# Kernel optimization log

Measured on AMD Instinct MI355X. Metric: run time of the kernel, lower is better.

The kernel has to match this reference:

```python
import jax, jax.numpy as jnp
import numpy as np

N_NODES = 100000
N_EDGES = 1600000
IN_SIZE = 512
HID_SIZE = 256
OUT_SIZE = 16
DROP_P = 0.5


def _degrees(idx, n):
    d = jax.ops.segment_sum(jnp.ones(idx.shape[0], jnp.float32), idx, num_segments=n)
    return jnp.maximum(d, 1.0)  # DGL clamps zero degrees to 1


def graph_conv(src, dst, feat, W, b, activation=None):
    # DGL GraphConv, norm='both': D_in^{-1/2} A D_out^{-1/2} X W + b
    n = feat.shape[0]
    inv_sqrt_dout = _degrees(src, n) ** -0.5   # out-degree of source nodes
    inv_sqrt_din = _degrees(dst, n) ** -0.5    # in-degree of destination nodes
    h = feat * inv_sqrt_dout[:, None]
    h = h @ W  # in_feats >= out_feats -> transform before aggregation (same math)
    # message passing: scatter-add source messages to destinations
    h = jax.ops.segment_sum(h[src], dst, num_segments=n)
    h = h * inv_sqrt_din[:, None] + b
    if activation is not None:
        h = activation(h)
    return h


def setup_inputs() -> dict:
    key = jax.random.key(0)
    ks = jax.random.split(key, 9)
    features = jax.random.normal(ks[0], (N_NODES, IN_SIZE), jnp.float32)
    src = jax.random.randint(ks[1], (N_EDGES,), 0, N_NODES)
    dst = jax.random.randint(ks[2], (N_EDGES,), 0, N_NODES)
    W1 = jax.random.normal(ks[3], (IN_SIZE, HID_SIZE), jnp.float32) / np.sqrt(IN_SIZE).astype(np.float32)
    b1 = jnp.zeros((HID_SIZE,), jnp.float32)
    W2 = jax.random.normal(ks[4], (HID_SIZE, HID_SIZE), jnp.float32) / np.sqrt(HID_SIZE).astype(np.float32)
    b2 = jnp.zeros((HID_SIZE,), jnp.float32)
    W3 = jax.random.normal(ks[5], (HID_SIZE, OUT_SIZE), jnp.float32) / np.sqrt(HID_SIZE).astype(np.float32)
    b3 = jnp.zeros((OUT_SIZE,), jnp.float32)
    return {"features": features, "src": src, "dst": dst,
            "W1": W1, "b1": b1, "W2": W2, "b2": b2, "W3": W3, "b3": b3}


def reference(features, src, dst, W1, b1, W2, b2, W3, b3):
    # layer 0: GraphConv + relu
    h = graph_conv(src, dst, features, W1, b1, activation=jax.nn.relu)
    # dropout(0.5) before layer 1 (deterministic fixed-key mask, training semantics)
    keep = jax.random.bernoulli(jax.random.key(42), 1.0 - DROP_P, h.shape)
    h = jnp.where(keep, h / (1.0 - DROP_P), 0.0)
    # layer 1: GraphConv (no activation)
    h = graph_conv(src, dst, h, W2, b2, activation=None)
    # layer 2: plain Linear head
    return h @ W3 + b3
```

## Files before the change

kernel.cpp:

```cpp
#include <hip/hip_runtime.h>
#include <stdint.h>

#define NN    100000
#define NE    1600000
#define IN_F  512
#define HID   256
#define OUTF  16
#define NPAD  100096
#define NBK   391
#define EPB   8192

typedef unsigned int u32;
typedef __bf16 bfrag  __attribute__((ext_vector_type(8)));
typedef float  f32x4  __attribute__((ext_vector_type(4)));
typedef short  s16x8  __attribute__((ext_vector_type(8)));

__device__ __forceinline__ u32 rotl32(u32 x, int r){ return (x<<r)|(x>>(32-r)); }

__device__ __forceinline__ bool drop_keep(u32 i){
    const u32 ks0 = 0u, ks1 = 42u, ks2 = 0x1BD11BDAu ^ 0u ^ 42u;
    u32 x0 = 0u + ks0;
    u32 x1 = i  + ks1;
#define TFR(r) { x0 += x1; x1 = rotl32(x1,(r)); x1 ^= x0; }
    TFR(13) TFR(15) TFR(26) TFR(6)   x0 += ks1; x1 += ks2 + 1u;
    TFR(17) TFR(29) TFR(16) TFR(24)  x0 += ks2; x1 += ks0 + 2u;
    TFR(13) TFR(15) TFR(26) TFR(6)   x0 += ks0; x1 += ks1 + 3u;
    TFR(17) TFR(29) TFR(16) TFR(24)  x0 += ks1; x1 += ks2 + 4u;
    TFR(13) TFR(15) TFR(26) TFR(6)   x0 += ks2; x1 += ks0 + 5u;
#undef TFR
    return ((x0 ^ x1) >> 31) == 0u;
}

__device__ __forceinline__ short f2b(float f){
    union { float f; u32 u; } v; v.f = f;
    u32 r = (v.u + 0x7FFFu + ((v.u >> 16) & 1u)) >> 16;
    return (short)r;
}
__device__ __forceinline__ float blo(u32 u){ union{u32 u; float f;} v; v.u = u << 16;         return v.f; }
__device__ __forceinline__ float bhi(u32 u){ union{u32 u; float f;} v; v.u = u & 0xFFFF0000u; return v.f; }

__device__ __forceinline__ u32 cvt_pk_bf16(float lo, float hi){
    u32 r;
    asm("v_cvt_pk_bf16_f32 %0, %1, %2" : "=v"(r) : "v"(lo), "v"(hi));
    return r;
}

__device__ __forceinline__ void gll16(const void* g, void* l){
    __builtin_amdgcn_global_load_lds((const __attribute__((address_space(1))) void*)g,
                                     (__attribute__((address_space(3))) void*)l, 16, 0, 0);
}


__global__ __launch_bounds__(256) void build_hist(const int4* __restrict__ src4,
                                                  const int4* __restrict__ dst4,
                                                  int* deg_out, int* __restrict__ bcnt){
    __shared__ int h[NBK];
    int t = threadIdx.x;
    for (int i = t; i < NBK; i += 256) h[i] = 0;
    __syncthreads();
    for (int i = blockIdx.x * 256 + t; i < NE / 4; i += gridDim.x * 256) {
        int4 s = src4[i];
        int4 d = dst4[i];
        atomicAdd(&deg_out[s.x], 1);
        atomicAdd(&deg_out[s.y], 1);
        atomicAdd(&deg_out[s.z], 1);
        atomicAdd(&deg_out[s.w], 1);
        atomicAdd(&h[d.x >> 8], 1);
        atomicAdd(&h[d.y >> 8], 1);
        atomicAdd(&h[d.z >> 8], 1);
        atomicAdd(&h[d.w >> 8], 1);
    }
    __syncthreads();
    for (int i = t; i < NBK; i += 256)
        if (h[i]) atomicAdd(&bcnt[i], h[i]);
}

__global__ __launch_bounds__(256) void finalize_deg(const int* __restrict__ deg_out,
                                                    const int* __restrict__ row_ptr,
                                                    float* isdo, float* isdi){
    int i = blockIdx.x * blockDim.x + threadIdx.x;
    if (i < NN) {
        isdo[i] = rsqrtf(fmaxf((float)deg_out[i], 1.0f));
        isdi[i] = rsqrtf(fmaxf((float)(row_ptr[i + 1] - row_ptr[i]), 1.0f));
    }
}

__global__ __launch_bounds__(512) void bucket_scan(const int* __restrict__ bcnt,
                                                   int* __restrict__ bbase,
                                                   int* __restrict__ bcur,
                                                   int* __restrict__ row_ptr){
    __shared__ int sh[512];
    int t = threadIdx.x;
    int v = (t < NBK) ? bcnt[t] : 0;
    sh[t] = v;
    __syncthreads();
    for (int off = 1; off < 512; off <<= 1) {
        int a = (t >= off) ? sh[t - off] : 0;
        __syncthreads();
        sh[t] += a;
        __syncthreads();
    }
    int excl = sh[t] - v;
    if (t < NBK) { bbase[t] = excl; bcur[t] = excl; }
    if (t == 0)  { bbase[NBK] = NE; row_ptr[NN] = NE; }
}

__global__ __launch_bounds__(256) void bucket_scatter(const int* __restrict__ src,
                                                      const int* __restrict__ dst,
                                                      int* bcur, u32* __restrict__ tmp){
    __shared__ int lh[NBK];
    __shared__ int lb[NBK];
    int t = threadIdx.x;
    for (int i = t; i < NBK; i += 256) lh[i] = 0;
    __syncthreads();
    const int e0 = blockIdx.x * EPB;
    for (int k = t * 4; k < EPB; k += 1024) {
        int e = e0 + k;
        if (e < NE) {
            int4 d = *(const int4*)(dst + e);
            atomicAdd(&lh[d.x >> 8], 1);
            atomicAdd(&lh[d.y >> 8], 1);
            atomicAdd(&lh[d.z >> 8], 1);
            atomicAdd(&lh[d.w >> 8], 1);
        }
    }
    __syncthreads();
    for (int i = t; i < NBK; i += 256) {
        int c = lh[i];
        if (c) lb[i] = atomicAdd(&bcur[i], c);
        lh[i] = 0;
    }
    __syncthreads();
    for (int k = t * 4; k < EPB; k += 1024) {
        int e = e0 + k;
        if (e < NE) {
            int4 d = *(const int4*)(dst + e);
            int4 s = *(const int4*)(src + e);
            int b0 = d.x >> 8, b1 = d.y >> 8, b2 = d.z >> 8, b3 = d.w >> 8;
            int r0 = atomicAdd(&lh[b0], 1);
            tmp[lb[b0] + r0] = ((u32)s.x << 8) | ((u32)d.x & 255u);
            int r1 = atomicAdd(&lh[b1], 1);
            tmp[lb[b1] + r1] = ((u32)s.y << 8) | ((u32)d.y & 255u);
            int r2 = atomicAdd(&lh[b2], 1);
            tmp[lb[b2] + r2] = ((u32)s.z << 8) | ((u32)d.z & 255u);
            int r3 = atomicAdd(&lh[b3], 1);
            tmp[lb[b3] + r3] = ((u32)s.w << 8) | ((u32)d.w & 255u);
        }
    }
}

__global__ __launch_bounds__(256) void bucket_finalize(const u32* __restrict__ tmp,
                                                       const int* __restrict__ bbase,
                                                       int* __restrict__ row_ptr,
                                                       int* __restrict__ col_src){
    __shared__ int h[256];
    __shared__ int wtot[4];
    const int t = threadIdx.x;
    const int b = blockIdx.x;
    const int base = bbase[b];
    const int cnt  = bbase[b + 1] - base;
    h[t] = 0;
    __syncthreads();
    for (int k = t; k < cnt; k += 256)
        atomicAdd(&h[tmp[base + k] & 255u], 1);
    __syncthreads();
    int v = h[t];
    int lane = t & 63, w = t >> 6;
    int s = v;
    #pragma unroll
    for (int off = 1; off < 64; off <<= 1) {
        int u = __shfl_up(s, off);
        if (lane >= off) s += u;
    }
    if (lane == 63) wtot[w] = s;
    __syncthreads();
    int woff = 0;
    #pragma unroll
    for (int i = 0; i < 4; ++i) woff += (i < w) ? wtot[i] : 0;
    int excl = woff + s - v;
    int d = (b << 8) + t;
    if (d < NN) row_ptr[d] = base + excl;
    h[t] = excl;
    __syncthreads();
    for (int k = t; k < cnt; k += 256) {
        u32 p = tmp[base + k];
        int r = atomicAdd(&h[p & 255u], 1);
        col_src[base + r] = (int)(p >> 8);
    }
}


template<int Kd, int Nd>
__global__ __launch_bounds__(256) void convert_wt(const float* __restrict__ W,
                                                  short* __restrict__ WT){
    int i = blockIdx.x * 256 + threadIdx.x;
    if (i >= Kd * Nd) return;
    int n = i / Kd, k = i - n * Kd;
    WT[i] = f2b(W[(size_t)k * Nd + n]);
}

__global__ __launch_bounds__(256) void gemm_x(const float* __restrict__ X,
                                              const short* __restrict__ BT,
                                              const float* __restrict__ isdo,
                                              short* __restrict__ C){
    __shared__ __align__(16) float As[4096];
    __shared__ __align__(16) short Bs[4096];

    const int t = threadIdx.x;
    const int wave = t >> 6, lane = t & 63;
    const int bm = blockIdx.x * 128;
    const int bn = blockIdx.y * 128;

    const int gsw = lane ^ ((lane >> 3) & 7);
    const int rl  = gsw >> 1;
    const int pp  = gsw & 1;
    const float* pa0 = X + (size_t)(((bm + 0*32 + rl) < NN) ? (bm + 0*32 + rl) : 0) * IN_F + wave * 8 + pp * 4;
    const float* pa1 = X + (size_t)(((bm + 1*32 + rl) < NN) ? (bm + 1*32 + rl) : 0) * IN_F + wave * 8 + pp * 4;
    const float* pa2 = X + (size_t)(((bm + 2*32 + rl) < NN) ? (bm + 2*32 + rl) : 0) * IN_F + wave * 8 + pp * 4;
    const float* pa3 = X + (size_t)(((bm + 3*32 + rl) < NN) ? (bm + 3*32 + rl) : 0) * IN_F + wave * 8 + pp * 4;
    float* lA = As + wave * 1024;

    const int ch0 = wave * 128 + lane;
    const int ch1 = ch0 + 64;
    const int kb0 = ch0 >> 7, r0 = ch0 & 127;
    const int kb1 = ch1 >> 7, r1 = ch1 & 127;
    const short* pb0 = BT + (size_t)(bn + r0) * IN_F + kb0 * 8;
    const short* pb1 = BT + (size_t)(bn + r1) * IN_F + kb1 * 8;
    short* lB0 = Bs + (size_t)(wave * 128) * 8;
    short* lB1 = Bs + (size_t)(wave * 128 + 64) * 8;

    const int wr = (wave >> 1) * 64, wc = (wave & 1) * 64;
    const int kq = lane >> 4, r15 = lane & 15;
    const short* fb = Bs + (size_t)(kq * 128 + wc + r15) * 8;

    f32x4 acc[4][4];
    #pragma unroll
    for (int m = 0; m < 4; ++m)
        #pragma unroll
        for (int n = 0; n < 4; ++n) acc[m][n] = (f32x4)0.0f;

    for (int k0 = 0; k0 < IN_F; k0 += 32) {
        gll16(pa0 + k0, lA);
        gll16(pa1 + k0, lA + 256);
        gll16(pa2 + k0, lA + 512);
        gll16(pa3 + k0, lA + 768);
        gll16(pb0 + k0, lB0);
        gll16(pb1 + k0, lB1);
        __syncthreads();

        bfrag af[4], bfg[4];
        #pragma unroll
        for (int m = 0; m < 4; ++m) {
            int r  = wr + m * 16 + r15;
            int j  = r >> 5, rr = r & 31;
            int g0 = 2 * rr;
            int G0 = g0 ^ ((g0 >> 3) & 7);
            int g1 = g0 + 1;
            int G1 = g1 ^ ((g1 >> 3) & 7);
            const float* base = As + kq * 1024 + j * 256;
            float4 f0 = *(const float4*)(base + G0 * 4);
            float4 f1 = *(const float4*)(base + G1 * 4);
            uint4 q = make_uint4(cvt_pk_bf16(f0.x, f0.y), cvt_pk_bf16(f0.z, f0.w),
                                 cvt_pk_bf16(f1.x, f1.y), cvt_pk_bf16(f1.z, f1.w));
            af[m] = *(bfrag*)&q;
        }
        #pragma unroll
        for (int n = 0; n < 4; ++n) bfg[n] = *(const bfrag*)(fb + n * 128);
        #pragma unroll
        for (int m = 0; m < 4; ++m)
            #pragma unroll
            for (int n = 0; n < 4; ++n)
                acc[m][n] = __builtin_amdgcn_mfma_f32_16x16x32_bf16(af[m], bfg[n], acc[m][n], 0, 0, 0);
        __syncthreads();
    }

    const int crow0 = bm + wr + (lane >> 4) * 4;
    const int ccol0 = bn + wc + (lane & 15);
    #pragma unroll
    for (int m = 0; m < 4; ++m)
        #pragma unroll
        for (int r = 0; r < 4; ++r) {
            int row = crow0 + m * 16 + r;
            float sc = (row < NN) ? isdo[row] : 0.0f;
            #pragma unroll
            for (int n = 0; n < 4; ++n)
                C[(size_t)row * HID + ccol0 + n * 16] = f2b(acc[m][n][r] * sc);
        }
}

template<int K>
__global__ __launch_bounds__(256) void gemm_bt(const short* __restrict__ A,
                                               const short* __restrict__ BT,
                                               short* __restrict__ C){
    __shared__ __align__(16) short As[4096];
    __shared__ __align__(16) short Bs[4096];

    const int t = threadIdx.x;
    const int wave = t >> 6, lane = t & 63;
    const int bm = blockIdx.x * 128;
    const int bn = blockIdx.y * 128;

    const int ch0 = wave * 128 + lane;
    const int ch1 = ch0 + 64;
    const int kb0 = ch0 >> 7, r0 = ch0 & 127;
    const int kb1 = ch1 >> 7, r1 = ch1 & 127;
    const short* pa0 = A  + (size_t)(bm + r0) * K + kb0 * 8;
    const short* pa1 = A  + (size_t)(bm + r1) * K + kb1 * 8;
    const short* pb0 = BT + (size_t)(bn + r0) * K + kb0 * 8;
    const short* pb1 = BT + (size_t)(bn + r1) * K + kb1 * 8;
    short* lA0 = As + (size_t)(wave * 128) * 8;
    short* lA1 = As + (size_t)(wave * 128 + 64) * 8;
    short* lB0 = Bs + (size_t)(wave * 128) * 8;
    short* lB1 = Bs + (size_t)(wave * 128 + 64) * 8;

    const int wr = (wave >> 1) * 64, wc = (wave & 1) * 64;
    const short* fa = As + (size_t)((lane >> 4) * 128 + wr + (lane & 15)) * 8;
    const short* fb = Bs + (size_t)((lane >> 4) * 128 + wc + (lane & 15)) * 8;

    f32x4 acc[4][4];
    #pragma unroll
    for (int m = 0; m < 4; ++m)
        #pragma unroll
        for (int n = 0; n < 4; ++n) acc[m][n] = (f32x4)0.0f;

    for (int k0 = 0; k0 < K; k0 += 32) {
        gll16(pa0 + k0, lA0);
        gll16(pa1 + k0, lA1);
        gll16(pb0 + k0, lB0);
        gll16(pb1 + k0, lB1);
        __syncthreads();

        bfrag af[4], bfg[4];
        #pragma unroll
        for (int m = 0; m < 4; ++m) af[m]  = *(const bfrag*)(fa + m * 128);
        #pragma unroll
        for (int n = 0; n < 4; ++n) bfg[n] = *(const bfrag*)(fb + n * 128);
        #pragma unroll
        for (int m = 0; m < 4; ++m)
            #pragma unroll
            for (int n = 0; n < 4; ++n)
                acc[m][n] = __builtin_amdgcn_mfma_f32_16x16x32_bf16(af[m], bfg[n], acc[m][n], 0, 0, 0);
        __syncthreads();
    }

    const int crow0 = bm + wr + (lane >> 4) * 4;
    const int ccol0 = bn + wc + (lane & 15);
    #pragma unroll
    for (int m = 0; m < 4; ++m)
        #pragma unroll
        for (int n = 0; n < 4; ++n)
            #pragma unroll
            for (int r = 0; r < 4; ++r)
                C[(size_t)(crow0 + m * 16 + r) * HID + ccol0 + n * 16] = f2b(acc[m][n][r]);
}

template<int MODE>
__global__ __launch_bounds__(256) void gather_agg(const short* __restrict__ H,
                                                  const int* __restrict__ rp,
                                                  const int* __restrict__ cs,
                                                  const float* __restrict__ isdi,
                                                  const float* __restrict__ isdo,
                                                  const float* __restrict__ bias,
                                                  short* __restrict__ out){
    const int lane = threadIdx.x & 63;
    const int node = __builtin_amdgcn_readfirstlane((int)(blockIdx.x * 4) + (int)(threadIdx.x >> 6));
    const int e0  = rp[node];
    const int end = rp[node + 1];
    const int sub = lane & 31, half = lane >> 5;
    const u32 off16 = (u32)sub * 16u;
    const char* Hb = (const char*)H;

    float a[8] = {0,0,0,0,0,0,0,0};
    float b[8] = {0,0,0,0,0,0,0,0};

#define LD4(s) (*(const uint4*)(Hb + ((((u32)(s)) << 9) | off16)))
#define ACC(A, u) { A[0]+=blo(u.x); A[1]+=bhi(u.x); A[2]+=blo(u.y); A[3]+=bhi(u.y); \
                    A[4]+=blo(u.z); A[5]+=bhi(u.z); A[6]+=blo(u.w); A[7]+=bhi(u.w); }

    int eb = e0;
    for (; eb + 16 <= end; eb += 16) {
        int t0 = cs[eb+0],  t1 = cs[eb+1],  t2 = cs[eb+2],  t3 = cs[eb+3];
        int t4 = cs[eb+4],  t5 = cs[eb+5],  t6 = cs[eb+6],  t7 = cs[eb+7];
        int t8 = cs[eb+8],  t9 = cs[eb+9],  tA = cs[eb+10], tB = cs[eb+11];
        int tC = cs[eb+12], tD = cs[eb+13], tE = cs[eb+14], tF = cs[eb+15];
        int s0 = half ? t1 : t0;
        int s1 = half ? t3 : t2;
        int s2 = half ? t5 : t4;
        int s3 = half ? t7 : t6;
        int s4 = half ? t9 : t8;
        int s5 = half ? tB : tA;
        int s6 = half ? tD : tC;
        int s7 = half ? tF : tE;
        uint4 u0 = LD4(s0), u1 = LD4(s1), u2 = LD4(s2), u3 = LD4(s3);
        uint4 u4 = LD4(s4), u5 = LD4(s5), u6 = LD4(s6), u7 = LD4(s7);
        ACC(a, u0); ACC(b, u1); ACC(a, u2); ACC(b, u3);
        ACC(a, u4); ACC(b, u5); ACC(a, u6); ACC(b, u7);
    }
    for (; eb + 8 <= end; eb += 8) {
        int t0 = cs[eb+0], t1 = cs[eb+1], t2 = cs[eb+2], t3 = cs[eb+3];
        int t4 = cs[eb+4], t5 = cs[eb+5], t6 = cs[eb+6], t7 = cs[eb+7];
        int s0 = half ? t1 : t0;
        int s1 = half ? t3 : t2;
        int s2 = half ? t5 : t4;
        int s3 = half ? t7 : t6;
        uint4 u0 = LD4(s0), u1 = LD4(s1), u2 = LD4(s2), u3 = LD4(s3);
        ACC(a, u0); ACC(b, u1); ACC(a, u2); ACC(b, u3);
    }
    for (; eb + 2 <= end; eb += 2) {
        int t0 = cs[eb], t1 = cs[eb+1];
        int s = half ? t1 : t0;
        uint4 u = LD4(s);
        ACC(a, u);
    }
    if (eb < end) {
        int s = cs[eb];
        uint4 u = LD4(s);
        if (half == 0) { ACC(a, u); }
    }
#undef ACC
#undef LD4
    #pragma unroll
    for (int j = 0; j < 8; ++j) a[j] += b[j];

    const int srcl = lane >> 1;
    const bool oddq = (lane & 1) != 0;
    float v[4];
    #pragma unroll
    for (int j = 0; j < 4; ++j) {
        float p0 = __shfl(a[j],     srcl);
        float p1 = __shfl(a[j + 4], srcl);
        float q0 = __shfl(a[j],     srcl + 32);
        float q1 = __shfl(a[j + 4], srcl + 32);
        v[j] = oddq ? (p1 + q1) : (p0 + q0);
    }

    float sd = isdi[node];
    float4 bb = *(const float4*)(bias + lane * 4);
    float h0 = v[0] * sd + bb.x;
    float h1 = v[1] * sd + bb.y;
    float h2 = v[2] * sd + bb.z;
    float h3 = v[3] * sd + bb.w;

    if (MODE == 0) {
        float so2 = 2.0f * isdo[node];
        u32 base = (u32)node * HID + (u32)lane * 4;
        h0 = drop_keep(base + 0) ? fmaxf(h0, 0.f) * so2 : 0.f;
        h1 = drop_keep(base + 1) ? fmaxf(h1, 0.f) * so2 : 0.f;
        h2 = drop_keep(base + 2) ? fmaxf(h2, 0.f) * so2 : 0.f;
        h3 = drop_keep(base + 3) ? fmaxf(h3, 0.f) * so2 : 0.f;
    }

    uint2 wv;
    wv.x = ((u32)(unsigned short)f2b(h1) << 16) | (u32)(unsigned short)f2b(h0);
    wv.y = ((u32)(unsigned short)f2b(h3) << 16) | (u32)(unsigned short)f2b(h2);
    *(uint2*)((char*)out + (size_t)node * 512 + (u32)lane * 8u) = wv;
}

__global__ __launch_bounds__(256) void head_kernel(const short* __restrict__ H2,
                                                   const float* __restrict__ W3,
                                                   const float* __restrict__ b3,
                                                   float* __restrict__ out){
    __shared__ float W3s[HID * OUTF];
    __shared__ short rows[16][HID + 8];
    int t = threadIdx.x;
    for (int i = t; i < HID * OUTF; i += 256) W3s[i] = W3[i];
    const int n0 = blockIdx.x * 16;
    for (int c = t; c < 16 * 32; c += 256) {
        int r = c >> 5, cc = c & 31;
        *(s16x8*)(&rows[r][cc * 8]) = *(const s16x8*)(H2 + (size_t)(n0 + r) * HID + cc * 8);
    }
    __syncthreads();
    int nl = t >> 4, k = t & 15;
    float acc = 0.0f;
    #pragma unroll 4
    for (int j = 0; j < HID; ++j)
        acc += blo((u32)(unsigned short)rows[nl][j]) * W3s[j * OUTF + k];
    out[(size_t)(n0 + nl) * OUTF + k] = acc + b3[k];
}

extern "C" void kernel_launch(void* const* d_in, const int* in_sizes, int n_in,
                              void* d_out, int out_size, void* d_ws, size_t ws_size,
                              hipStream_t stream) {
    const float* X   = (const float*)d_in[0];
    const int*   src = (const int*)  d_in[1];
    const int*   dst = (const int*)  d_in[2];
    const float* W1  = (const float*)d_in[3];
    const float* b1  = (const float*)d_in[4];
    const float* W2  = (const float*)d_in[5];
    const float* b2  = (const float*)d_in[6];
    const float* W3  = (const float*)d_in[7];
    const float* b3  = (const float*)d_in[8];
    float* out = (float*)d_out;

    char* ws = (char*)d_ws;
    size_t o = 0;
    int*   deg_out = (int*)  (ws + o); o += (size_t)NN * 4;
    int*   bcnt    = (int*)  (ws + o); o += (size_t)NBK * 4;
    float* isdo    = (float*)(ws + o); o += (size_t)NN * 4;
    float* isdi    = (float*)(ws + o); o += (size_t)NN * 4;
    int*   row_ptr = (int*)  (ws + o); o += (size_t)(NN + 1) * 4;
    int*   bbase   = (int*)  (ws + o); o += (size_t)(NBK + 1) * 4;
    int*   bcur    = (int*)  (ws + o); o += (size_t)NBK * 4;
    int*   col_src = (int*)  (ws + o); o += (size_t)NE * 4;
    o = (o + 255) & ~(size_t)255;
    short* W1t = (short*)(ws + o); o += (size_t)IN_F * HID * 2;
    short* W2t = (short*)(ws + o); o += (size_t)HID * HID * 2;
    o = (o + 255) & ~(size_t)255;
    short* hA    = (short*)(ws + o); o += (size_t)NPAD * HID * 2;
    short* hB    = (short*)(ws + o); o += (size_t)NPAD * HID * 2;
    short* h2pre = (short*)(ws + o); o += (size_t)NPAD * HID * 2;
    if (ws_size < o) return;
    short* h2  = hA;
    u32*   tmp = (u32*)hB;

    const size_t zlen = (size_t)NN * 4 + (size_t)NBK * 4;
    hipMemsetAsync(deg_out, 0, zlen, stream);

    build_hist<<<256, 256, 0, stream>>>((const int4*)src, (const int4*)dst, deg_out, bcnt);
    bucket_scan<<<1, 512, 0, stream>>>(bcnt, bbase, bcur, row_ptr);
    bucket_scatter<<<(NE + EPB - 1) / EPB, 256, 0, stream>>>(src, dst, bcur, tmp);
    bucket_finalize<<<NBK, 256, 0, stream>>>(tmp, bbase, row_ptr, col_src);
    finalize_deg<<<(NN + 255) / 256, 256, 0, stream>>>(deg_out, row_ptr, isdo, isdi);

    convert_wt<IN_F, HID><<<IN_F * HID / 256, 256, 0, stream>>>(W1, W1t);
    convert_wt<HID, HID><<<HID * HID / 256, 256, 0, stream>>>(W2, W2t);

    dim3 ggrid(NPAD / 128, 2);

    gemm_x<<<ggrid, 256, 0, stream>>>(X, W1t, isdo, hA);
    gather_agg<0><<<NN / 4, 256, 0, stream>>>(hA, row_ptr, col_src, isdi, isdo, b1, hB);

    gemm_bt<HID><<<ggrid, 256, 0, stream>>>(hB, W2t, h2pre);
    gather_agg<1><<<NN / 4, 256, 0, stream>>>(h2pre, row_ptr, col_src, isdi, isdo, b2, h2);

    head_kernel<<<NN / 16, 256, 0, stream>>>(h2, W3, b3, out);
}
```

Measured before the change: 535.7 us.

## Double-buffer LDS tiles in both GEMM kernels to overlap loads with MFMA

Both GEMM kernels now use two LDS buffers. The next K-tile's global-to-LDS loads are issued before the current tile is computed, and a partial vmcnt wait plus raw barriers replace the full __syncthreads. The goal is to hide global load latency behind the MFMA work. In exchange, LDS use per block doubles (48KB for gemm_x), which may reduce occupancy, and correctness depends on the hand-written vmcnt counts matching the number of outstanding loads.

New measurement: 538.3 us. Within noise of the previous version (+0.5%).

```diff
diff --git a/kernel.cpp b/kernel.cpp
--- a/kernel.cpp
+++ b/kernel.cpp
@@ -203,8 +203,8 @@
                                               const short* __restrict__ BT,
                                               const float* __restrict__ isdo,
                                               short* __restrict__ C){
-    __shared__ __align__(16) float As[4096];
-    __shared__ __align__(16) short Bs[4096];
+    __shared__ __align__(16) float As[2 * 4096];
+    __shared__ __align__(16) short Bs[2 * 4096];
 
     const int t = threadIdx.x;
     const int wave = t >> 6, lane = t & 63;
@@ -218,7 +218,6 @@
     const float* pa1 = X + (size_t)(((bm + 1*32 + rl) < NN) ? (bm + 1*32 + rl) : 0) * IN_F + wave * 8 + pp * 4;
     const float* pa2 = X + (size_t)(((bm + 2*32 + rl) < NN) ? (bm + 2*32 + rl) : 0) * IN_F + wave * 8 + pp * 4;
     const float* pa3 = X + (size_t)(((bm + 3*32 + rl) < NN) ? (bm + 3*32 + rl) : 0) * IN_F + wave * 8 + pp * 4;
-    float* lA = As + wave * 1024;
 
     const int ch0 = wave * 128 + lane;
     const int ch1 = ch0 + 64;
@@ -226,12 +225,9 @@
     const int kb1 = ch1 >> 7, r1 = ch1 & 127;
     const short* pb0 = BT + (size_t)(bn + r0) * IN_F + kb0 * 8;
     const short* pb1 = BT + (size_t)(bn + r1) * IN_F + kb1 * 8;
-    short* lB0 = Bs + (size_t)(wave * 128) * 8;
-    short* lB1 = Bs + (size_t)(wave * 128 + 64) * 8;
 
     const int wr = (wave >> 1) * 64, wc = (wave & 1) * 64;
     const int kq = lane >> 4, r15 = lane & 15;
-    const short* fb = Bs + (size_t)(kq * 128 + wc + r15) * 8;
 
     f32x4 acc[4][4];
     #pragma unroll
@@ -239,40 +235,56 @@
         #pragma unroll
         for (int n = 0; n < 4; ++n) acc[m][n] = (f32x4)0.0f;
 
-    for (int k0 = 0; k0 < IN_F; k0 += 32) {
-        gll16(pa0 + k0, lA);
-        gll16(pa1 + k0, lA + 256);
-        gll16(pa2 + k0, lA + 512);
-        gll16(pa3 + k0, lA + 768);
-        gll16(pb0 + k0, lB0);
-        gll16(pb1 + k0, lB1);
-        __syncthreads();
-
-        bfrag af[4], bfg[4];
-        #pragma unroll
-        for (int m = 0; m < 4; ++m) {
-            int r  = wr + m * 16 + r15;
-            int j  = r >> 5, rr = r & 31;
-            int g0 = 2 * rr;
-            int G0 = g0 ^ ((g0 >> 3) & 7);
-            int g1 = g0 + 1;
-            int G1 = g1 ^ ((g1 >> 3) & 7);
-            const float* base = As + kq * 1024 + j * 256;
-            float4 f0 = *(const float4*)(base + G0 * 4);
-            float4 f1 = *(const float4*)(base + G1 * 4);
-            uint4 q = make_uint4(cvt_pk_bf16(f0.x, f0.y), cvt_pk_bf16(f0.z, f0.w),
-                                 cvt_pk_bf16(f1.x, f1.y), cvt_pk_bf16(f1.z, f1.w));
-            af[m] = *(bfrag*)&q;
-        }
-        #pragma unroll
-        for (int n = 0; n < 4; ++n) bfg[n] = *(const bfrag*)(fb + n * 128);
-        #pragma unroll
-        for (int m = 0; m < 4; ++m)
-            #pragma unroll
-            for (int n = 0; n < 4; ++n)
-                acc[m][n] = __builtin_amdgcn_mfma_f32_16x16x32_bf16(af[m], bfg[n], acc[m][n], 0, 0, 0);
-        __syncthreads();
-    }
+#define STAGE_X(BUF, K0) { \
+    float* lA = As + (BUF) * 4096 + wave * 1024; \
+    gll16(pa0 + (K0), lA);       gll16(pa1 + (K0), lA + 256); \
+    gll16(pa2 + (K0), lA + 512); gll16(pa3 + (K0), lA + 768); \
+    short* lb = Bs + (BUF) * 4096 + (size_t)(wave * 128) * 8; \
+    gll16(pb0 + (K0), lb);       gll16(pb1 + (K0), lb + 512); }
+
+#define COMPUTE_X(BUF) { \
+    const float* AsC = As + (BUF) * 4096; \
+    const short* BsC = Bs + (BUF) * 4096; \
+    const short* fbC = BsC + (size_t)(kq * 128 + wc + r15) * 8; \
+    bfrag af[4], bfg[4]; \
+    _Pragma("unroll") \
+    for (int m = 0; m < 4; ++m) { \
+        int r  = wr + m * 16 + r15; \
+        int j  = r >> 5, rr = r & 31; \
+        int g0 = 2 * rr;  int G0 = g0 ^ ((g0 >> 3) & 7); \
+        int g1 = g0 + 1;  int G1 = g1 ^ ((g1 >> 3) & 7); \
+        const float* base = AsC + kq * 1024 + j * 256; \
+        float4 f0 = *(const float4*)(base + G0 * 4); \
+        float4 f1 = *(const float4*)(base + G1 * 4); \
+        uint4 q = make_uint4(cvt_pk_bf16(f0.x, f0.y), cvt_pk_bf16(f0.z, f0.w), \
+                             cvt_pk_bf16(f1.x, f1.y), cvt_pk_bf16(f1.z, f1.w)); \
+        af[m] = *(bfrag*)&q; \
+    } \
+    _Pragma("unroll") \
+    for (int n = 0; n < 4; ++n) bfg[n] = *(const bfrag*)(fbC + n * 128); \
+    _Pragma("unroll") \
+    for (int m = 0; m < 4; ++m) \
+        _Pragma("unroll") \
+        for (int n = 0; n < 4; ++n) \
+            acc[m][n] = __builtin_amdgcn_mfma_f32_16x16x32_bf16(af[m], bfg[n], acc[m][n], 0, 0, 0); }
+
+    const int NT = IN_F / 32;
+    STAGE_X(0, 0);
+    int cur = 0;
+    for (int tt = 0; tt < NT - 1; ++tt) {
+        STAGE_X(cur ^ 1, (tt + 1) * 32);
+        asm volatile("s_waitcnt vmcnt(6)" ::: "memory");
+        __builtin_amdgcn_s_barrier();
+        COMPUTE_X(cur);
+        asm volatile("" ::: "memory");
+        __builtin_amdgcn_s_barrier();
+        cur ^= 1;
+    }
+    asm volatile("s_waitcnt vmcnt(0)" ::: "memory");
+    __builtin_amdgcn_s_barrier();
+    COMPUTE_X(cur);
+#undef STAGE_X
+#undef COMPUTE_X
 
     const int crow0 = bm + wr + (lane >> 4) * 4;
     const int ccol0 = bn + wc + (lane & 15);
@@ -292,8 +304,8 @@
 __global__ __launch_bounds__(256) void gemm_bt(const short* __restrict__ A,
                                                const short* __restrict__ BT,
                                                short* __restrict__ C){
-    __shared__ __align__(16) short As[4096];
-    __shared__ __align__(16) short Bs[4096];
+    __shared__ __align__(16) short As[2 * 4096];
+    __shared__ __align__(16) short Bs[2 * 4096];
 
     const int t = threadIdx.x;
     const int wave = t >> 6, lane = t & 63;
@@ -308,14 +320,9 @@
     const short* pa1 = A  + (size_t)(bm + r1) * K + kb1 * 8;
     const short* pb0 = BT + (size_t)(bn + r0) * K + kb0 * 8;
     const short* pb1 = BT + (size_t)(bn + r1) * K + kb1 * 8;
-    short* lA0 = As + (size_t)(wave * 128) * 8;
-    short* lA1 = As + (size_t)(wave * 128 + 64) * 8;
-    short* lB0 = Bs + (size_t)(wave * 128) * 8;
-    short* lB1 = Bs + (size_t)(wave * 128 + 64) * 8;
 
     const int wr = (wave >> 1) * 64, wc = (wave & 1) * 64;
-    const short* fa = As + (size_t)((lane >> 4) * 128 + wr + (lane & 15)) * 8;
-    const short* fb = Bs + (size_t)((lane >> 4) * 128 + wc + (lane & 15)) * 8;
+    const int frag_off = ((lane >> 4) * 128 + (lane & 15)) * 8;
 
     f32x4 acc[4][4];
     #pragma unroll
@@ -323,25 +330,43 @@
         #pragma unroll
         for (int n = 0; n < 4; ++n) acc[m][n] = (f32x4)0.0f;
 
-    for (int k0 = 0; k0 < K; k0 += 32) {
-        gll16(pa0 + k0, lA0);
-        gll16(pa1 + k0, lA1);
-        gll16(pb0 + k0, lB0);
-        gll16(pb1 + k0, lB1);
-        __syncthreads();
-
-        bfrag af[4], bfg[4];
-        #pragma unroll
-        for (int m = 0; m < 4; ++m) af[m]  = *(const bfrag*)(fa + m * 128);
-        #pragma unroll
-        for (int n = 0; n < 4; ++n) bfg[n] = *(const bfrag*)(fb + n * 128);
-        #pragma unroll
-        for (int m = 0; m < 4; ++m)
-            #pragma unroll
-            for (int n = 0; n < 4; ++n)
-                acc[m][n] = __builtin_amdgcn_mfma_f32_16x16x32_bf16(af[m], bfg[n], acc[m][n], 0, 0, 0);
-        __syncthreads();
-    }
+#define STAGE_B(BUF, K0) { \
+    short* la = As + (BUF) * 4096 + (size_t)(wave * 128) * 8; \
+    short* lb = Bs + (BUF) * 4096 + (size_t)(wave * 128) * 8; \
+    gll16(pa0 + (K0), la); gll16(pa1 + (K0), la + 512); \
+    gll16(pb0 + (K0), lb); gll16(pb1 + (K0), lb + 512); }
+
+#define COMPUTE_B(BUF) { \
+    const short* fa = As + (BUF) * 4096 + frag_off + wr * 8; \
+    const short* fb = Bs + (BUF) * 4096 + frag_off + wc * 8; \
+    bfrag af[4], bfg[4]; \
+    _Pragma("unroll") \
+    for (int m = 0; m < 4; ++m) af[m]  = *(const bfrag*)(fa + m * 128); \
+    _Pragma("unroll") \
+    for (int n = 0; n < 4; ++n) bfg[n] = *(const bfrag*)(fb + n * 128); \
+    _Pragma("unroll") \
+    for (int m = 0; m < 4; ++m) \
+        _Pragma("unroll") \
+        for (int n = 0; n < 4; ++n) \
+            acc[m][n] = __builtin_amdgcn_mfma_f32_16x16x32_bf16(af[m], bfg[n], acc[m][n], 0, 0, 0); }
+
+    const int NT = K / 32;
+    STAGE_B(0, 0);
+    int cur = 0;
+    for (int tt = 0; tt < NT - 1; ++tt) {
+        STAGE_B(cur ^ 1, (tt + 1) * 32);
+        asm volatile("s_waitcnt vmcnt(4)" ::: "memory");
+        __builtin_amdgcn_s_barrier();
+        COMPUTE_B(cur);
+        asm volatile("" ::: "memory");
+        __builtin_amdgcn_s_barrier();
+        cur ^= 1;
+    }
+    asm volatile("s_waitcnt vmcnt(0)" ::: "memory");
+    __builtin_amdgcn_s_barrier();
+    COMPUTE_B(cur);
+#undef STAGE_B
+#undef COMPUTE_B
 
     const int crow0 = bm + wr + (lane >> 4) * 4;
     const int ccol0 = bn + wc + (lane & 15);
```
